# Kernel tuning notes

Hardware: AMD Instinct MI355X
Metric: run time of the kernel (lower is better)

The kernel has to match this reference:

```python
import jax, jax.numpy as jnp
import numpy as np
import math

N, D, H = 4096, 2048, 16
HD = D // H  # head_dim = 128


def setup_inputs() -> dict:
    key = jax.random.key(0)
    ks = jax.random.split(key, 9)
    s = 1.0 / math.sqrt(D)
    return {
        "x":  jax.random.normal(ks[0], (N, D), dtype=jnp.float32),
        "Wq": jax.random.normal(ks[1], (D, D), dtype=jnp.float32) * s,
        "bq": jax.random.normal(ks[2], (D,), dtype=jnp.float32) * s,
        "Wk": jax.random.normal(ks[3], (D, D), dtype=jnp.float32) * s,
        "bk": jax.random.normal(ks[4], (D,), dtype=jnp.float32) * s,
        "Wv": jax.random.normal(ks[5], (D, D), dtype=jnp.float32) * s,
        "bv": jax.random.normal(ks[6], (D,), dtype=jnp.float32) * s,
        "Wo": jax.random.normal(ks[7], (D, D), dtype=jnp.float32) * s,
        "bo": jax.random.normal(ks[8], (D,), dtype=jnp.float32) * s,
    }


def reference(x, Wq, bq, Wk, bk, Wv, bv, Wo, bo):
    # eqx.nn.Linear: y = W @ x + b, weight shape (out, in) -> x @ W.T + b
    q = x @ Wq.T + bq            # [N, D]
    k = x @ Wk.T + bk            # [N, D]
    v = x @ Wv.T + bv            # [N, D]
    q = q.reshape(N, H, HD).transpose(1, 0, 2)   # [H, N, hd]
    k = k.reshape(N, H, HD).transpose(1, 2, 0)   # [H, hd, N]
    v = v.reshape(N, H, HD).transpose(1, 0, 2)   # [H, N, hd]
    scale = 1.0 / math.sqrt(HD)
    scores = jnp.matmul(q * scale, k)            # [H, N, N]
    attn = jax.nn.softmax(scores, axis=-1)
    ctx = jnp.matmul(attn, v)                    # [H, N, hd]
    ctx = ctx.transpose(1, 0, 2).reshape(N, D)   # [N, D]
    return ctx @ Wo.T + bo
```

## Files before the change

### kernel.cpp

```cpp
#include <hip/hip_runtime.h>
#include <stdint.h>

#define N_TOK 4096
#define DIM   2048
#define NH    16
#define HD    128
#define NW    (DIM * DIM)

using bf16x8 = __attribute__((ext_vector_type(8))) short;
using bf16x4 = __attribute__((ext_vector_type(4))) short;
using f32x4  = __attribute__((ext_vector_type(4))) float;
using u32x2  = __attribute__((ext_vector_type(2))) unsigned int;

#if __has_builtin(__builtin_amdgcn_exp2f)
#define EXP2(x) __builtin_amdgcn_exp2f(x)
#else
#define EXP2(x) exp2f(x)
#endif

__device__ inline unsigned short f2bf(float f) {
  union { float f; unsigned u; } v; v.f = f;
  unsigned r = v.u + 0x7FFFu + ((v.u >> 16) & 1u);
  return (unsigned short)(r >> 16);
}
__device__ inline float bf2f(unsigned short u) {
  union { unsigned u; float f; } v; v.u = ((unsigned)u) << 16; return v.f;
}
__device__ inline f32x4 mfma16(bf16x8 a, bf16x8 b, f32x4 c) {
  return __builtin_amdgcn_mfma_f32_16x16x32_bf16(a, b, c, 0, 0, 0);
}
__device__ inline void gll16(const unsigned short* g, unsigned short* l) {
  __builtin_amdgcn_global_load_lds(
      (const __attribute__((address_space(1))) void*)g,
      (__attribute__((address_space(3))) void*)l, 16, 0, 0);
}
__device__ inline void wgbar() {
  asm volatile("" ::: "memory");
  __builtin_amdgcn_s_barrier();
  asm volatile("" ::: "memory");
}

__device__ inline unsigned cvtpk_bf16(float lo, float hi) {
  unsigned r;
  asm("v_cvt_pk_bf16_f32 %0, %1, %2" : "=v"(r) : "v"(lo), "v"(hi));
  return r;
}

__device__ inline u32x2 pl32swap(unsigned a, unsigned b) {
#if __has_builtin(__builtin_amdgcn_permlane32_swap)
  return __builtin_amdgcn_permlane32_swap(a, b, false, false);
#else
  int lane = threadIdx.x & 63;
  unsigned as = (unsigned)__shfl_xor((int)a, 32);
  unsigned bs = (unsigned)__shfl_xor((int)b, 32);
  u32x2 r;
  r.x = (lane & 32) ? bs : a;
  r.y = (lane & 32) ? b : as;
  return r;
#endif
}
__device__ inline u32x2 pl16swap(unsigned a, unsigned b) {
#if __has_builtin(__builtin_amdgcn_permlane16_swap)
  return __builtin_amdgcn_permlane16_swap(a, b, false, false);
#else
  int lane = threadIdx.x & 63;
  unsigned as = (unsigned)__shfl_xor((int)a, 16);
  unsigned bs = (unsigned)__shfl_xor((int)b, 16);
  u32x2 r;
  r.x = (lane & 16) ? bs : a;
  r.y = (lane & 16) ? b : as;
  return r;
#endif
}

__global__ __launch_bounds__(256)
void cvt_bf16(const float* __restrict__ src, unsigned short* __restrict__ dst, int n) {
  int i = blockIdx.x * 256 + threadIdx.x;
  if (i * 8 >= n) return;
  const float4* s = (const float4*)src + (size_t)i * 2;
  float4 a = s[0], b = s[1];
  bf16x8 o;
  o[0] = (short)f2bf(a.x); o[1] = (short)f2bf(a.y);
  o[2] = (short)f2bf(a.z); o[3] = (short)f2bf(a.w);
  o[4] = (short)f2bf(b.x); o[5] = (short)f2bf(b.y);
  o[6] = (short)f2bf(b.z); o[7] = (short)f2bf(b.w);
  *(bf16x8*)(dst + (size_t)i * 8) = o;
}

template<int OUT_MODE>
__global__ __launch_bounds__(512, 2)
void gemm_bf16(const unsigned short* __restrict__ A, const unsigned short* __restrict__ B,
               const float* __restrict__ bias, void* __restrict__ out_, float scale) {
  constexpr int BM = 256, BN = 128, BK = 64;
  constexpr int NKT = DIM / BK;
  __shared__ unsigned short Asl[3][BM * BK];
  __shared__ unsigned short Bsl[3][BN * BK];

  const int tid  = threadIdx.x;
  const int lane = tid & 63;
  const int w    = tid >> 6;
  const int wm = w >> 1, wn = w & 1;
  const int lr = lane & 15, quad = lane >> 4;

  const int bid = blockIdx.x;
  const int nb  = (bid & 7) * 32 + (bid >> 3);
  const int m0  = (nb >> 4) * BM;
  const int n0  = (nb & 15) * BN;

  const f32x4 vzero = {0.f, 0.f, 0.f, 0.f};
  f32x4 acc[4][4];
#pragma unroll
  for (int i = 0; i < 4; ++i)
#pragma unroll
    for (int j = 0; j < 4; ++j) acc[i][j] = vzero;

  size_t asrc[4]; int aldst[4];
  size_t bsrc[2]; int bldst[2];
#pragma unroll
  for (int i = 0; i < 4; ++i) {
    int ch = tid + i * 512;
    int row = ch >> 3, cc = ch & 7;
    int gcc = cc ^ (row & 7);
    asrc[i]  = (size_t)(m0 + row) * DIM + gcc * 8;
    aldst[i] = ch * 8;
  }
#pragma unroll
  for (int i = 0; i < 2; ++i) {
    int ch = tid + i * 512;
    int row = ch >> 3, cc = ch & 7;
    int gcc = cc ^ (row & 7);
    bsrc[i]  = (size_t)(n0 + row) * DIM + gcc * 8;
    bldst[i] = ch * 8;
  }
  auto stage_all = [&](int buf, int k0) {
    gll16(&A[asrc[0] + k0], &Asl[buf][aldst[0]]);
    gll16(&A[asrc[1] + k0], &Asl[buf][aldst[1]]);
    gll16(&A[asrc[2] + k0], &Asl[buf][aldst[2]]);
    gll16(&A[asrc[3] + k0], &Asl[buf][aldst[3]]);
    gll16(&B[bsrc[0] + k0], &Bsl[buf][bldst[0]]);
    gll16(&B[bsrc[1] + k0], &Bsl[buf][bldst[1]]);
  };

  auto lda = [&](int buf, int ks, bf16x8* af) {
#pragma unroll
    for (int mb = 0; mb < 4; ++mb) {
      int row  = wm * 64 + mb * 16 + lr;
      int slot = (ks * 4 + quad) ^ (row & 7);
      af[mb] = *(const bf16x8*)&Asl[buf][row * 64 + slot * 8];
    }
  };
  auto ldb = [&](int buf, int ks, bf16x8* bfv) {
#pragma unroll
    for (int nb2 = 0; nb2 < 4; ++nb2) {
      int row  = wn * 64 + nb2 * 16 + lr;
      int slot = (ks * 4 + quad) ^ (row & 7);
      bfv[nb2] = *(const bf16x8*)&Bsl[buf][row * 64 + slot * 8];
    }
  };
  auto mm = [&](bf16x8* af, bf16x8* bfv) {
    __builtin_amdgcn_s_setprio(1);
#pragma unroll
    for (int mb = 0; mb < 4; ++mb)
#pragma unroll
      for (int nb2 = 0; nb2 < 4; ++nb2)
        acc[mb][nb2] = mfma16(af[mb], bfv[nb2], acc[mb][nb2]);
    __builtin_amdgcn_s_setprio(0);
  };

  stage_all(0, 0);
  stage_all(1, BK);
  asm volatile("s_waitcnt vmcnt(6)" ::: "memory");
  wgbar();

  for (int t = 0; t < NKT - 2; ++t) {
    const int buf = t % 3, sb = (t + 2) % 3, sk = (t + 2) * BK;
    bf16x8 af[4], bfv[4];
    lda(buf, 0, af); ldb(buf, 0, bfv);
    stage_all(sb, sk);
    wgbar();
    mm(af, bfv);
    lda(buf, 1, af); ldb(buf, 1, bfv);
    mm(af, bfv);
    asm volatile("s_waitcnt vmcnt(6)" ::: "memory");
    wgbar();
  }
  {
    const int buf = (NKT - 2) % 3;
    bf16x8 af[4], bfv[4];
    lda(buf, 0, af); ldb(buf, 0, bfv);
    wgbar();
    mm(af, bfv);
    lda(buf, 1, af); ldb(buf, 1, bfv);
    mm(af, bfv);
    asm volatile("s_waitcnt vmcnt(0)" ::: "memory");
    wgbar();
  }
  {
    const int buf = (NKT - 1) % 3;
    bf16x8 af[4], bfv[4];
    lda(buf, 0, af); ldb(buf, 0, bfv);
    mm(af, bfv);
    lda(buf, 1, af); ldb(buf, 1, bfv);
    mm(af, bfv);
  }

#pragma unroll
  for (int mb = 0; mb < 4; ++mb)
#pragma unroll
    for (int nb2 = 0; nb2 < 4; ++nb2) {
      int gn = n0 + wn * 64 + nb2 * 16 + lr;
      int gm_base = m0 + wm * 64 + mb * 16 + quad * 4;
      float bs = bias[gn];
      if constexpr (OUT_MODE == 2) {
        bf16x4 pk;
#pragma unroll
        for (int r = 0; r < 4; ++r) pk[r] = (short)f2bf((acc[mb][nb2][r] + bs) * scale);
        *(bf16x4*)&((unsigned short*)out_)[(size_t)gn * N_TOK + gm_base] = pk;
      } else {
#pragma unroll
        for (int r = 0; r < 4; ++r) {
          float v = (acc[mb][nb2][r] + bs) * scale;
          if constexpr (OUT_MODE == 1)
            ((float*)out_)[(size_t)(gm_base + r) * DIM + gn] = v;
          else
            ((unsigned short*)out_)[(size_t)(gm_base + r) * DIM + gn] = f2bf(v);
        }
      }
    }
}

__global__ __launch_bounds__(256, 1)
void flash_attn(const unsigned short* __restrict__ Q,
                const unsigned short* __restrict__ K,
                const unsigned short* __restrict__ Vt,
                unsigned short* __restrict__ ctx) {
  constexpr int LDK = 136;
  constexpr int LDV = 72;
  constexpr int NT  = N_TOK / 64;
  __shared__ unsigned short Ksl[64 * LDK];
  __shared__ unsigned short VTsl[128 * LDV];

  const int tid  = threadIdx.x;
  const int lane = tid & 63, w = tid >> 6;
  const int lr = lane & 15, quad = lane >> 4;

  const int bid  = blockIdx.x;
  const int head = (bid & 7) * 2 + ((bid >> 3) & 1);
  const int qblk = bid >> 4;
  const int hoff = head * HD;
  const int q0   = qblk * 256;
  const int qw   = q0 + w * 64;

  bf16x8 qf[4][4];
#pragma unroll
  for (int mb = 0; mb < 4; ++mb)
#pragma unroll
    for (int c = 0; c < 4; ++c)
      qf[mb][c] = *(const bf16x8*)&Q[(size_t)(qw + mb * 16 + lr) * DIM + hoff + c * 32 + quad * 8];

  const f32x4 vzero = {0.f, 0.f, 0.f, 0.f};
  f32x4 o[4][8];
  float l_acc[4] = {0.f, 0.f, 0.f, 0.f};
#pragma unroll
  for (int mb = 0; mb < 4; ++mb)
#pragma unroll
    for (int nb = 0; nb < 8; ++nb) o[mb][nb] = vzero;

  bf16x8 kreg[4], vreg[4];
  auto load_tile = [&](int kt) {
    int kbase = kt * 64;
#pragma unroll
    for (int i = 0; i < 4; ++i) {
      int ch = tid + i * 256;
      kreg[i] = *(const bf16x8*)&K[(size_t)(kbase + (ch >> 4)) * DIM + hoff + (ch & 15) * 8];
      vreg[i] = *(const bf16x8*)&Vt[(size_t)(hoff + (ch >> 3)) * N_TOK + kbase + (ch & 7) * 8];
    }
  };
  load_tile(0);

  for (int kt = 0; kt < NT; ++kt) {
    __syncthreads();
#pragma unroll
    for (int i = 0; i < 4; ++i) {
      int ch = tid + i * 256;
      *(bf16x8*)&Ksl[(ch >> 4) * LDK + (ch & 15) * 8] = kreg[i];
      *(bf16x8*)&VTsl[(ch >> 3) * LDV + (ch & 7) * 8] = vreg[i];
    }
    __syncthreads();
    if (kt + 1 < NT) load_tile(kt + 1);

    f32x4 s[4][4];
#pragma unroll
    for (int mb = 0; mb < 4; ++mb)
#pragma unroll
      for (int nf = 0; nf < 4; ++nf) s[mb][nf] = vzero;
#pragma unroll
    for (int nf = 0; nf < 4; ++nf)
#pragma unroll
      for (int c = 0; c < 4; ++c) {
        bf16x8 kf = *(const bf16x8*)&Ksl[(nf * 16 + lr) * LDK + c * 32 + quad * 8];
#pragma unroll
        for (int mb = 0; mb < 4; ++mb) s[mb][nf] = mfma16(kf, qf[mb][c], s[mb][nf]);
      }

    bf16x8 pf[4][2];
#pragma unroll
    for (int mb = 0; mb < 4; ++mb) {
      unsigned W[4][2];
      float lp = 0.f;
#pragma unroll
      for (int nf = 0; nf < 4; ++nf) {
        float e0 = EXP2(s[mb][nf][0]);
        float e1 = EXP2(s[mb][nf][1]);
        float e2 = EXP2(s[mb][nf][2]);
        float e3 = EXP2(s[mb][nf][3]);
        lp += (e0 + e1) + (e2 + e3);
        W[nf][0] = cvtpk_bf16(e0, e1);
        W[nf][1] = cvtpk_bf16(e2, e3);
      }
      l_acc[mb] += lp;
#pragma unroll
      for (int ki = 0; ki < 2; ++ki) {
        u32x2 a0  = pl32swap(W[2 * ki][0], W[2 * ki + 1][0]);
        u32x2 t02 = pl16swap(a0.x, a0.y);
        u32x2 a1  = pl32swap(W[2 * ki][1], W[2 * ki + 1][1]);
        u32x2 t13 = pl16swap(a1.x, a1.y);
        union { unsigned u[4]; bf16x8 v; } pu;
        pu.u[0] = t02.x; pu.u[1] = t13.x; pu.u[2] = t02.y; pu.u[3] = t13.y;
        pf[mb][ki] = pu.v;
      }
    }

#pragma unroll
    for (int nb = 0; nb < 8; ++nb)
#pragma unroll
      for (int ki = 0; ki < 2; ++ki) {
        bf16x8 vf = *(const bf16x8*)&VTsl[(nb * 16 + lr) * LDV + ki * 32 + quad * 8];
#pragma unroll
        for (int mb = 0; mb < 4; ++mb) o[mb][nb] = mfma16(pf[mb][ki], vf, o[mb][nb]);
      }
  }

#pragma unroll
  for (int mb = 0; mb < 4; ++mb) {
    float t = l_acc[mb];
    t += __shfl_xor(t, 16);
    t += __shfl_xor(t, 32);
    l_acc[mb] = t;
  }
#pragma unroll
  for (int mb = 0; mb < 4; ++mb)
#pragma unroll
    for (int r = 0; r < 4; ++r) {
      float Lr = __shfl(l_acc[mb], quad * 4 + r);
      float inv = 1.0f / Lr;
      int gq = qw + mb * 16 + quad * 4 + r;
#pragma unroll
      for (int nb = 0; nb < 8; ++nb)
        ctx[(size_t)gq * DIM + hoff + nb * 16 + lr] = f2bf(o[mb][nb][r] * inv);
    }
}

extern "C" void kernel_launch(void* const* d_in, const int* in_sizes, int n_in,
                              void* d_out, int out_size, void* d_ws, size_t ws_size,
                              hipStream_t stream) {
  (void)in_sizes; (void)n_in; (void)out_size; (void)ws_size;
  const float* x  = (const float*)d_in[0];
  const float* Wq = (const float*)d_in[1];
  const float* bq = (const float*)d_in[2];
  const float* Wk = (const float*)d_in[3];
  const float* bk = (const float*)d_in[4];
  const float* Wv = (const float*)d_in[5];
  const float* bv = (const float*)d_in[6];
  const float* Wo = (const float*)d_in[7];
  const float* bo = (const float*)d_in[8];

  const size_t NE = (size_t)N_TOK * DIM;
  unsigned short* xb  = (unsigned short*)d_ws;
  unsigned short* Wqb = xb + NE;
  unsigned short* Wkb = Wqb + NW;
  unsigned short* Wvb = Wkb + NW;
  unsigned short* Wob = Wvb + NW;
  unsigned short* Qb  = Wob + NW;
  unsigned short* Kb  = Qb + NE;
  unsigned short* Vtb = Kb + NE;

  cvt_bf16<<<4096, 256, 0, stream>>>(x,  xb,  (int)NE);
  cvt_bf16<<<2048, 256, 0, stream>>>(Wq, Wqb, NW);
  cvt_bf16<<<2048, 256, 0, stream>>>(Wk, Wkb, NW);
  cvt_bf16<<<2048, 256, 0, stream>>>(Wv, Wvb, NW);
  cvt_bf16<<<2048, 256, 0, stream>>>(Wo, Wob, NW);

  const float qscale = 1.4426950408889634f * 0.08838834764831845f;

  gemm_bf16<0><<<256, 512, 0, stream>>>(xb, Wqb, bq, Qb, qscale);
  gemm_bf16<0><<<256, 512, 0, stream>>>(xb, Wkb, bk, Kb, 1.0f);
  gemm_bf16<2><<<256, 512, 0, stream>>>(xb, Wvb, bv, Vtb, 1.0f);

  unsigned short* ctxb = xb;
  flash_attn<<<256, 256, 0, stream>>>(Qb, Kb, Vtb, ctxb);

  gemm_bf16<1><<<256, 512, 0, stream>>>(ctxb, Wob, bo, (float*)d_out, 1.0f);
}
```

Baseline: 453.4 us.

## Shrink GEMM tile to 128x128 with 256 threads and double buffering

Changes the projection GEMMs from 256x128 tiles with 512 threads and a triple-buffered LDS pipeline to 128x128 tiles with 256 threads and double buffering. The grid doubles to 512 blocks to cover more CUs and cut LDS use per block. In exchange each tile gets less data reuse, and the pipeline now waits on vmcnt(0) and adds barriers every iteration, which exposes more global-load latency.

```diff
diff --git a/kernel.cpp b/kernel.cpp
--- a/kernel.cpp
+++ b/kernel.cpp
@@ -88,13 +88,13 @@
 }
 
 template<int OUT_MODE>
-__global__ __launch_bounds__(512, 2)
+__global__ __launch_bounds__(256, 2)
 void gemm_bf16(const unsigned short* __restrict__ A, const unsigned short* __restrict__ B,
                const float* __restrict__ bias, void* __restrict__ out_, float scale) {
-  constexpr int BM = 256, BN = 128, BK = 64;
+  constexpr int BM = 128, BN = 128, BK = 64;
   constexpr int NKT = DIM / BK;
-  __shared__ unsigned short Asl[3][BM * BK];
-  __shared__ unsigned short Bsl[3][BN * BK];
+  __shared__ unsigned short Asl[2][BM * BK];
+  __shared__ unsigned short Bsl[2][BN * BK];
 
   const int tid  = threadIdx.x;
   const int lane = tid & 63;
@@ -103,7 +103,7 @@
   const int lr = lane & 15, quad = lane >> 4;
 
   const int bid = blockIdx.x;
-  const int nb  = (bid & 7) * 32 + (bid >> 3);
+  const int nb  = (bid & 7) * 64 + (bid >> 3);
   const int m0  = (nb >> 4) * BM;
   const int n0  = (nb & 15) * BN;
 
@@ -115,30 +115,22 @@
     for (int j = 0; j < 4; ++j) acc[i][j] = vzero;
 
   size_t asrc[4]; int aldst[4];
-  size_t bsrc[2]; int bldst[2];
+  size_t bsrc[4]; int bldst[4];
 #pragma unroll
   for (int i = 0; i < 4; ++i) {
-    int ch = tid + i * 512;
+    int ch = tid + i * 256;
     int row = ch >> 3, cc = ch & 7;
     int gcc = cc ^ (row & 7);
     asrc[i]  = (size_t)(m0 + row) * DIM + gcc * 8;
     aldst[i] = ch * 8;
-  }
-#pragma unroll
-  for (int i = 0; i < 2; ++i) {
-    int ch = tid + i * 512;
-    int row = ch >> 3, cc = ch & 7;
-    int gcc = cc ^ (row & 7);
     bsrc[i]  = (size_t)(n0 + row) * DIM + gcc * 8;
     bldst[i] = ch * 8;
   }
   auto stage_all = [&](int buf, int k0) {
-    gll16(&A[asrc[0] + k0], &Asl[buf][aldst[0]]);
-    gll16(&A[asrc[1] + k0], &Asl[buf][aldst[1]]);
-    gll16(&A[asrc[2] + k0], &Asl[buf][aldst[2]]);
-    gll16(&A[asrc[3] + k0], &Asl[buf][aldst[3]]);
-    gll16(&B[bsrc[0] + k0], &Bsl[buf][bldst[0]]);
-    gll16(&B[bsrc[1] + k0], &Bsl[buf][bldst[1]]);
+#pragma unroll
+    for (int i = 0; i < 4; ++i) gll16(&A[asrc[i] + k0], &Asl[buf][aldst[i]]);
+#pragma unroll
+    for (int i = 0; i < 4; ++i) gll16(&B[bsrc[i] + k0], &Bsl[buf][bldst[i]]);
   };
 
   auto lda = [&](int buf, int ks, bf16x8* af) {
@@ -168,35 +160,25 @@
   };
 
   stage_all(0, 0);
-  stage_all(1, BK);
-  asm volatile("s_waitcnt vmcnt(6)" ::: "memory");
+  asm volatile("s_waitcnt vmcnt(0)" ::: "memory");
   wgbar();
 
-  for (int t = 0; t < NKT - 2; ++t) {
-    const int buf = t % 3, sb = (t + 2) % 3, sk = (t + 2) * BK;
+  for (int t = 0; t < NKT - 1; ++t) {
+    const int buf = t & 1, sk = (t + 1) * BK;
     bf16x8 af[4], bfv[4];
     lda(buf, 0, af); ldb(buf, 0, bfv);
-    stage_all(sb, sk);
+    stage_all(buf ^ 1, sk);
     wgbar();
     mm(af, bfv);
+    wgbar();
     lda(buf, 1, af); ldb(buf, 1, bfv);
-    mm(af, bfv);
-    asm volatile("s_waitcnt vmcnt(6)" ::: "memory");
-    wgbar();
-  }
-  {
-    const int buf = (NKT - 2) % 3;
-    bf16x8 af[4], bfv[4];
-    lda(buf, 0, af); ldb(buf, 0, bfv);
+    asm volatile("s_waitcnt vmcnt(0)" ::: "memory");
     wgbar();
     mm(af, bfv);
-    lda(buf, 1, af); ldb(buf, 1, bfv);
-    mm(af, bfv);
-    asm volatile("s_waitcnt vmcnt(0)" ::: "memory");
     wgbar();
   }
   {
-    const int buf = (NKT - 1) % 3;
+    const int buf = (NKT - 1) & 1;
     bf16x8 af[4], bfv[4];
     lda(buf, 0, af); ldb(buf, 0, bfv);
     mm(af, bfv);
@@ -393,12 +375,12 @@
 
   const float qscale = 1.4426950408889634f * 0.08838834764831845f;
 
-  gemm_bf16<0><<<256, 512, 0, stream>>>(xb, Wqb, bq, Qb, qscale);
-  gemm_bf16<0><<<256, 512, 0, stream>>>(xb, Wkb, bk, Kb, 1.0f);
-  gemm_bf16<2><<<256, 512, 0, stream>>>(xb, Wvb, bv, Vtb, 1.0f);
+  gemm_bf16<0><<<512, 256, 0, stream>>>(xb, Wqb, bq, Qb, qscale);
+  gemm_bf16<0><<<512, 256, 0, stream>>>(xb, Wkb, bk, Kb, 1.0f);
+  gemm_bf16<2><<<512, 256, 0, stream>>>(xb, Wvb, bv, Vtb, 1.0f);
 
   unsigned short* ctxb = xb;
   flash_attn<<<256, 256, 0, stream>>>(Qb, Kb, Vtb, ctxb);
 
-  gemm_bf16<1><<<256, 512, 0, stream>>>(ctxb, Wob, bo, (float*)d_out, 1.0f);
-}
+  gemm_bf16<1><<<512, 256, 0, stream>>>(ctxb, Wob, bo, (float*)d_out, 1.0f);
+}
```

Result: faster. 442.4 us (median of 2 runs) (-2.4%).
